# Kernel tuning notes

Hardware: AMD Instinct MI355X
Metric: run time of the kernel (lower is better)

## Reference

```python
import jax, jax.numpy as jnp
import numpy as np
from jax import lax

N = 1_000_000   # nodes
E = 16_000_000  # edges
K1, K2, K3 = 100_000, 10_000, 2_500  # ceil(ratio*n) per pooling stage
EPS = 1e-5


def cgconv(x, src, dst, edge_attr, edge_valid, Wf, bf, Ws, bs, gamma, beta, num_nodes):
    # z_ij = [x_i, x_j, e_ij]  (PyG: i = target = dst, j = source = src)
    z = jnp.concatenate([x[dst], x[src], edge_attr], axis=-1)          # [E,3]
    m = jax.nn.sigmoid(z @ Wf + bf) * jax.nn.softplus(z @ Ws + bs)     # [E,1]
    m = m * edge_valid[:, None].astype(m.dtype)
    aggr = jax.ops.segment_sum(m, dst, num_segments=num_nodes)         # [n,1]
    # BatchNorm1d (training-mode batch stats, biased var), then residual
    mean = aggr.mean(axis=0)
    var = aggr.var(axis=0)
    bn = gamma * (aggr - mean) / jnp.sqrt(var + EPS) + beta
    return bn + x


def topk_pool(x, src, dst, edge_attr, edge_valid, w, k, num_nodes):
    # Original torch code broadcasts x[N,1]*w[C] -> sum(-1) == x*sum(w); tanh nonlinearity.
    score = jnp.tanh(x[:, 0] * jnp.sum(w) / jnp.linalg.norm(w))        # [n]
    top_scores, perm = lax.top_k(score, k)
    x_new = x[perm] * top_scores[:, None]
    mask = jnp.zeros((num_nodes,), bool).at[perm].set(True)
    new_idx = jnp.zeros((num_nodes,), jnp.int32).at[perm].set(jnp.arange(k, dtype=jnp.int32))
    ev = edge_valid & mask[src] & mask[dst]
    return x_new, new_idx[src], new_idx[dst], edge_attr, ev


def setup_inputs() -> dict:
    key = jax.random.key(0)
    ks = jax.random.split(key, 24)
    d = {}
    d["x"] = jax.random.normal(ks[0], (N, 1), jnp.float32)
    d["edge_attr"] = jax.random.uniform(ks[1], (E, 1), jnp.float32)
    d["src"] = jax.random.randint(ks[2], (E,), 0, N, jnp.int32)
    d["dst"] = jax.random.randint(ks[3], (E,), 0, N, jnp.int32)
    d["batch"] = jnp.zeros((N,), jnp.int32)
    p = lambda k, shp: jax.random.normal(k, shp, jnp.float32) * 0.1
    d["Wf1"], d["bf1"] = p(ks[4], (3, 1)), p(ks[5], (1,))
    d["Ws1"], d["bs1"] = p(ks[6], (3, 1)), p(ks[7], (1,))
    d["g1"], d["be1"] = jnp.ones((1,), jnp.float32), jnp.zeros((1,), jnp.float32)
    d["Wf2"], d["bf2"] = p(ks[8], (3, 1)), p(ks[9], (1,))
    d["Ws2"], d["bs2"] = p(ks[10], (3, 1)), p(ks[11], (1,))
    d["g2"], d["be2"] = jnp.ones((1,), jnp.float32), jnp.zeros((1,), jnp.float32)
    d["pw1"] = p(ks[12], (800,))
    d["pw2"] = p(ks[13], (80,))
    d["pw3"] = p(ks[14], (8,))
    d["Wl1"], d["bl1"] = p(ks[15], (1, 8)), p(ks[16], (8,))
    d["Wl2"], d["bl2"] = p(ks[17], (8, 2)), p(ks[18], (2,))
    return d


def reference(x, edge_attr, Wf1, bf1, Ws1, bs1, g1, be1, Wf2, bf2, Ws2, bs2, g2, be2,
              pw1, pw2, pw3, Wl1, bl1, Wl2, bl2, src, dst, batch):
    ev = jnp.ones((E,), bool)
    x = cgconv(x, src, dst, edge_attr, ev, Wf1, bf1, Ws1, bs1, g1, be1, N)
    x, s, dd, ea, ev = topk_pool(x, src, dst, edge_attr, ev, pw1, K1, N)
    x = cgconv(x, s, dd, ea, ev, Wf2, bf2, Ws2, bs2, g2, be2, K1)
    x, s, dd, ea, ev = topk_pool(x, s, dd, ea, ev, pw2, K2, K1)
    x, s, dd, ea, ev = topk_pool(x, s, dd, ea, ev, pw3, K3, K2)
    h = jax.nn.relu(x @ Wl1 + bl1)
    # dropout is identity in eval/reference mode
    return jax.nn.log_softmax(h @ Wl2 + bl2, axis=1)
```

## Files before the change

### kernel.cpp

```cpp
#include <hip/hip_runtime.h>
#include <math.h>

#define CHUNK 4096
#define NB2   256
#define BSH   12
#define CAP   20
#define CAPW  41
#define FG    16
#define RND   1024
#define EPB   16384

typedef int      i32x4 __attribute__((ext_vector_type(4)));
typedef float    f32x4 __attribute__((ext_vector_type(4)));
typedef unsigned u32x2 __attribute__((ext_vector_type(2)));
typedef unsigned u32x4 __attribute__((ext_vector_type(4)));

__device__ __forceinline__ i32x4 ntld4i(const int* p)   { return __builtin_nontemporal_load((const i32x4*)p); }
__device__ __forceinline__ f32x4 ntld4f(const float* p) { return __builtin_nontemporal_load((const f32x4*)p); }

__device__ __forceinline__ float sigmoidf_(float x) {
    if (x >= 0.0f) { float e = expf(-x); return 1.0f / (1.0f + e); }
    float e = expf(x); return e / (1.0f + e);
}
__device__ __forceinline__ float softplusf_(float x) {
    return fmaxf(x, 0.0f) + log1pf(expf(-fabsf(x)));
}
__device__ __forceinline__ unsigned key_desc(float f) {
    unsigned u = __float_as_uint(f);
    unsigned ka = (u & 0x80000000u) ? ~u : (u | 0x80000000u);
    return ~ka;
}
__device__ __forceinline__ float edge_m(float xd, float xs, float a,
                                        float wf0, float wf1, float wf2, float b0,
                                        float ws0, float ws1, float ws2, float b1) {
    float f = xd * wf0 + xs * wf1 + a * wf2 + b0;
    float g = xd * ws0 + xs * ws1 + a * ws2 + b1;
    return sigmoidf_(f) * softplusf_(g);
}

__global__ void k_consts(const float* __restrict__ pw1, const float* __restrict__ pw2,
                         const float* __restrict__ pw3, float* __restrict__ consts,
                         float* __restrict__ stats, unsigned* __restrict__ ghist,
                         int n1, int n2, int n3) {
    if (blockIdx.x == 0) {
        if (threadIdx.x < 16) stats[threadIdx.x] = 0.f;
        for (int i = threadIdx.x; i < 2048; i += 256) ghist[i] = 0u;
    }
    const float* w; int n;
    if (blockIdx.x == 0)      { w = pw1; n = n1; }
    else if (blockIdx.x == 1) { w = pw2; n = n2; }
    else                      { w = pw3; n = n3; }
    __shared__ float s1[256], s2[256];
    float a = 0.f, b = 0.f;
    for (int i = threadIdx.x; i < n; i += 256) { float v = w[i]; a += v; b += v * v; }
    s1[threadIdx.x] = a; s2[threadIdx.x] = b; __syncthreads();
    for (int o = 128; o > 0; o >>= 1) {
        if (threadIdx.x < o) { s1[threadIdx.x] += s1[threadIdx.x + o]; s2[threadIdx.x] += s2[threadIdx.x + o]; }
        __syncthreads();
    }
    if (threadIdx.x == 0) consts[blockIdx.x] = s1[0] / sqrtf(s2[0]);
}

__global__ void __launch_bounds__(256) k_ehist2(const int* __restrict__ dst,
                                                unsigned* __restrict__ hist,
                                                int e0, int e1) {
    __shared__ unsigned h[NB2];
    int t = threadIdx.x;
    h[t] = 0;
    __syncthreads();
    int cs = e0 + blockIdx.x * EPB;
    int ce = cs + EPB; if (ce > e1) ce = e1;
    for (int eb = cs; eb < ce; eb += RND) {
        int i = eb + t * 4;
        if (eb + RND <= ce) {
            i32x4 d4 = ntld4i(dst + i);
            atomicAdd(&h[((unsigned)d4.x) >> BSH], 1u);
            atomicAdd(&h[((unsigned)d4.y) >> BSH], 1u);
            atomicAdd(&h[((unsigned)d4.z) >> BSH], 1u);
            atomicAdd(&h[((unsigned)d4.w) >> BSH], 1u);
        } else {
            #pragma unroll
            for (int j = 0; j < 4; ++j)
                if (i + j < ce) atomicAdd(&h[((unsigned)dst[i + j]) >> BSH], 1u);
        }
    }
    __syncthreads();
    hist[(size_t)blockIdx.x * NB2 + t] = h[t];
}

__global__ void k_scanA(const unsigned* __restrict__ hist, unsigned* __restrict__ offs,
                        unsigned* __restrict__ tot, int G, unsigned rmask) {
    int d = blockIdx.x, ND = gridDim.x, t = threadIdx.x;
    __shared__ unsigned s[256];
    unsigned carry = 0;
    for (int tile = 0; tile * 256 < G; ++tile) {
        int g = tile * 256 + t;
        unsigned v = (g < G) ? ((hist[(size_t)g * ND + d] + rmask) & ~rmask) : 0u;
        s[t] = v; __syncthreads();
        for (int o = 1; o < 256; o <<= 1) {
            unsigned u = (t >= o) ? s[t - o] : 0u;
            __syncthreads();
            s[t] += u; __syncthreads();
        }
        if (g < G) offs[(size_t)g * ND + d] = s[t] - v + carry;
        unsigned tl = s[255]; __syncthreads();
        carry += tl;
    }
    if (t == 0) tot[d] = carry;
}

__global__ void __launch_bounds__(256) k_part(
        const float* __restrict__ x, const float* __restrict__ ea,
        const int* __restrict__ src, const int* __restrict__ dst,
        const float* __restrict__ Wf, const float* __restrict__ bf,
        const float* __restrict__ Ws, const float* __restrict__ bs,
        const unsigned* __restrict__ offs, const unsigned* __restrict__ tot,
        const unsigned* __restrict__ eh,
        uint2* __restrict__ rec, int e0, int e1) {
    __shared__ unsigned stage[NB2 * CAPW];
    __shared__ unsigned gcur[NB2], fil[NB2], gend[NB2];
    __shared__ unsigned short wl[2][NB2];
    __shared__ unsigned wlc[2];
    int t = threadIdx.x;
    {
        unsigned v = tot[t];
        stage[t] = v; __syncthreads();
        for (int o = 1; o < 256; o <<= 1) {
            unsigned u = (t >= o) ? stage[t - o] : 0u;
            __syncthreads();
            stage[t] += u; __syncthreads();
        }
        unsigned g0 = (stage[t] - v) + offs[(size_t)blockIdx.x * NB2 + t];
        unsigned cnt = eh[(size_t)blockIdx.x * NB2 + t];
        gcur[t] = g0;
        gend[t] = g0 + ((cnt + FG - 1) & ~(unsigned)(FG - 1));
        fil[t] = 0;
        if (t < 2) wlc[t] = 0;
    }
    __syncthreads();
    int cs = e0 + blockIdx.x * EPB;
    int ce = cs + EPB; if (ce > e1) ce = e1;
    float wf0 = Wf[0], wf1 = Wf[1], wf2 = Wf[2], b0 = bf[0];
    float ws0 = Ws[0], ws1 = Ws[1], ws2 = Ws[2], b1 = bs[0];
    int sg = t >> 4, ln = t & 15;
    int rnd = 0;
    for (int rb = cs; rb < ce; rb += RND, ++rnd) {
        int cur = rnd & 1;
        int s4[4], d4[4]; float a4[4]; bool vl[4];
        int eb = rb + t * 4;
        if (rb + RND <= ce) {
            i32x4 sv = ntld4i(src + eb);
            i32x4 dv = ntld4i(dst + eb);
            f32x4 av = ntld4f(ea + eb);
            s4[0]=sv.x; s4[1]=sv.y; s4[2]=sv.z; s4[3]=sv.w;
            d4[0]=dv.x; d4[1]=dv.y; d4[2]=dv.z; d4[3]=dv.w;
            a4[0]=av.x; a4[1]=av.y; a4[2]=av.z; a4[3]=av.w;
            vl[0]=vl[1]=vl[2]=vl[3]=true;
        } else {
            #pragma unroll
            for (int j = 0; j < 4; ++j) {
                int e = eb + j;
                vl[j] = e < ce;
                s4[j] = vl[j] ? src[e] : 0;
                d4[j] = vl[j] ? dst[e] : 0;
                a4[j] = vl[j] ? ea[e]  : 0.f;
            }
        }
        #pragma unroll
        for (int j = 0; j < 4; ++j) {
            if (!vl[j]) continue;
            int d = d4[j];
            float m = edge_m(x[d], x[s4[j]], a4[j], wf0, wf1, wf2, b0, ws0, ws1, ws2, b1);
            unsigned bin = ((unsigned)d) >> BSH;
            unsigned dl  = (unsigned)(d & ((1 << BSH) - 1));
            unsigned slot = atomicAdd(&fil[bin], 1u);
            if (slot == FG - 1) {
                unsigned w = atomicAdd(&wlc[cur], 1u);
                wl[cur][w] = (unsigned short)bin;
            }
            if (slot < CAP) {
                stage[bin * CAPW + 2 * slot]     = __float_as_uint(m);
                stage[bin * CAPW + 2 * slot + 1] = dl;
            } else {
                rec[gcur[bin] + slot] = make_uint2(__float_as_uint(m), dl);
            }
        }
        __syncthreads();
        unsigned nw = wlc[cur];
        for (unsigned i = sg; i < nw; i += 16) {
            int b = wl[cur][i];
            unsigned c = fil[b], g = gcur[b];
            unsigned* st = &stage[b * CAPW];
            if (c > CAP) {
                rec[g + ln] = make_uint2(st[2 * ln], st[2 * ln + 1]);
                if (ln < CAP - 16)
                    rec[g + 16 + ln] = make_uint2(st[2 * (16 + ln)], st[2 * (16 + ln) + 1]);
                if (ln == 0) { gcur[b] = g + c; fil[b] = 0; }
            } else {
                rec[g + ln] = make_uint2(st[2 * ln], st[2 * ln + 1]);
                unsigned rem = c - FG;
                unsigned a0 = 0, a1 = 0;
                if (ln < rem) { a0 = st[2 * (FG + ln)]; a1 = st[2 * (FG + ln) + 1]; }
                if (ln < rem) { st[2 * ln] = a0; st[2 * ln + 1] = a1; }
                if (ln == 0) { gcur[b] = g + FG; fil[b] = rem; }
            }
        }
        if (t == 0) wlc[cur ^ 1] = 0;
        __syncthreads();
    }
    for (int i = 0; i < NB2 / 16; ++i) {
        int b = sg + (i << 4);
        unsigned g = gcur[b], c = fil[b], ge = gend[b];
        unsigned* st = &stage[b * CAPW];
        for (unsigned p = g + ln; p < ge; p += 16) {
            unsigned k2 = p - g;
            rec[p] = (k2 < c) ? make_uint2(st[2 * k2], st[2 * k2 + 1]) : make_uint2(0u, 0u);
        }
    }
}

__global__ void __launch_bounds__(256) k_aggr2(
        const uint2* __restrict__ rec, const unsigned* __restrict__ tot,
        float* __restrict__ aggr, float* __restrict__ stats,
        int N, int accumulate, int doStats) {
    __shared__ float acc[1 << BSH];
    __shared__ unsigned sc[256];
    __shared__ unsigned sBase, sCnt;
    int t = threadIdx.x, b = blockIdx.x;
    {
        unsigned v = tot[t];
        sc[t] = v; __syncthreads();
        for (int o = 1; o < 256; o <<= 1) {
            unsigned u = (t >= o) ? sc[t - o] : 0u;
            __syncthreads();
            sc[t] += u; __syncthreads();
        }
        if (t == b) { sBase = sc[t] - v; sCnt = tot[t]; }
    }
    for (int i = t; i < (1 << BSH); i += 256) acc[i] = 0.f;
    __syncthreads();
    unsigned lo = sBase, hi = lo + sCnt;
    for (unsigned i = lo + 2 * t; i < hi; i += 512) {
        u32x4 r = __builtin_nontemporal_load((const u32x4*)&rec[i]);
        atomicAdd(&acc[r.y], __uint_as_float(r.x));
        atomicAdd(&acc[r.w], __uint_as_float(r.z));
    }
    __syncthreads();
    int nb = b << BSH;
    float s = 0.f, q = 0.f;
    for (int i = t; i < (1 << BSH); i += 256) {
        int node = nb + i;
        if (node < N) {
            float v = acc[i];
            if (accumulate) v += aggr[node];
            aggr[node] = v;
            if (doStats) { s += v; q += v * v; }
        }
    }
    if (doStats) {
        __shared__ float s1[256], s2[256];
        s1[t] = s; s2[t] = q; __syncthreads();
        for (int o = 128; o > 0; o >>= 1) {
            if (t < o) { s1[t] += s1[t + o]; s2[t] += s2[t + o]; }
            __syncthreads();
        }
        if (t == 0) { atomicAdd(&stats[0], s1[0]); atomicAdd(&stats[1], s2[0]); }
    }
}

__global__ void k_conv1(const float* __restrict__ x, const float* __restrict__ ea,
                        const int* __restrict__ src, const int* __restrict__ dst,
                        const float* __restrict__ Wf, const float* __restrict__ bf,
                        const float* __restrict__ Ws, const float* __restrict__ bs,
                        float* __restrict__ aggr, int E) {
    int e = blockIdx.x * blockDim.x + threadIdx.x;
    if (e >= E) return;
    int s = src[e], d = dst[e];
    atomicAdd(&aggr[d], edge_m(x[d], x[s], ea[e], Wf[0], Wf[1], Wf[2], bf[0],
                               Ws[0], Ws[1], Ws[2], bs[0]));
}

__global__ void __launch_bounds__(256) k_conv2(
        const float* __restrict__ x2, const float* __restrict__ ea,
        const int* __restrict__ src, const int* __restrict__ dst,
        const int* __restrict__ nidx,
        const float* __restrict__ Wf, const float* __restrict__ bf,
        const float* __restrict__ Ws, const float* __restrict__ bs,
        float* __restrict__ aggr, int E) {
    int base = (blockIdx.x * 256 + threadIdx.x) * 4;
    if (base >= E) return;
    float wf0 = Wf[0], wf1 = Wf[1], wf2 = Wf[2], b0 = bf[0];
    float ws0 = Ws[0], ws1 = Ws[1], ws2 = Ws[2], b1 = bs[0];
    int d4[4], s4[4]; int cnt;
    if (base + 4 <= E) {
        i32x4 dv = ntld4i(dst + base);
        i32x4 sv = ntld4i(src + base);
        d4[0]=dv.x; d4[1]=dv.y; d4[2]=dv.z; d4[3]=dv.w;
        s4[0]=sv.x; s4[1]=sv.y; s4[2]=sv.z; s4[3]=sv.w;
        cnt = 4;
    } else {
        cnt = E - base;
        for (int j = 0; j < cnt; ++j) { d4[j] = dst[base + j]; s4[j] = src[base + j]; }
    }
    #pragma unroll
    for (int j = 0; j < 4; ++j) {
        if (j >= cnt) break;
        int nd = nidx[d4[j]];
        if (nd < 0) continue;
        int ns = nidx[s4[j]];
        if (ns < 0) continue;
        float a = __builtin_nontemporal_load(ea + base + j);
        atomicAdd(&aggr[nd], edge_m(x2[nd], x2[ns], a, wf0, wf1, wf2, b0, ws0, ws1, ws2, b1));
    }
}

__global__ void k_stats(const float* __restrict__ a, int n, float* __restrict__ stats) {
    float s = 0.f, q = 0.f;
    int stride = gridDim.x * blockDim.x;
    for (int i = blockIdx.x * blockDim.x + threadIdx.x; i < n; i += stride) {
        float v = a[i]; s += v; q += v * v;
    }
    __shared__ float s1[256], s2[256];
    s1[threadIdx.x] = s; s2[threadIdx.x] = q; __syncthreads();
    for (int o = 128; o > 0; o >>= 1) {
        if (threadIdx.x < o) { s1[threadIdx.x] += s1[threadIdx.x + o]; s2[threadIdx.x] += s2[threadIdx.x + o]; }
        __syncthreads();
    }
    if (threadIdx.x == 0) { atomicAdd(&stats[0], s1[0]); atomicAdd(&stats[1], s2[0]); }
}

__global__ void k_bn(const float* __restrict__ aggr, const float* __restrict__ xin,
                     const float* __restrict__ stats, const float* __restrict__ g,
                     const float* __restrict__ be, float* __restrict__ xout,
                     int n, float invn, const float* __restrict__ consts, int ci,
                     unsigned* __restrict__ keys, unsigned* __restrict__ vals,
                     int* __restrict__ nidxInit, float* __restrict__ zeroArr, int nZero) {
    int i = blockIdx.x * blockDim.x + threadIdx.x;
    if (i >= n) return;
    if (nidxInit) nidxInit[i] = -1;
    if (zeroArr && i < nZero) zeroArr[i] = 0.f;
    float mean = stats[0] * invn;
    float var  = stats[1] * invn - mean * mean;
    float inv  = 1.0f / sqrtf(var + 1e-5f);
    float v = g[0] * (aggr[i] - mean) * inv + be[0] + xin[i];
    xout[i] = v;
    float s = tanhf(v * consts[ci]);
    keys[i] = key_desc(s);
    vals[i] = (unsigned)i;
}

__global__ void __launch_bounds__(256) k_ghist(const unsigned* __restrict__ keys,
                                               unsigned* __restrict__ ghist, int n) {
    __shared__ unsigned h[2048];
    int t = threadIdx.x;
    for (int i = t; i < 2048; i += 256) h[i] = 0;
    __syncthreads();
    int stride = gridDim.x * 1024;
    for (int base = blockIdx.x * 1024 + t * 4; base + 3 < n; base += stride) {
        u32x4 k4 = __builtin_nontemporal_load((const u32x4*)(keys + base));
        atomicAdd(&h[k4.x >> 21], 1u);
        atomicAdd(&h[k4.y >> 21], 1u);
        atomicAdd(&h[k4.z >> 21], 1u);
        atomicAdd(&h[k4.w >> 21], 1u);
    }
    if (blockIdx.x == 0) {
        int tail = n & ~3;
        for (int i = tail + t; i < n; i += 256)
            atomicAdd(&h[keys[i] >> 21], 1u);
    }
    __syncthreads();
    for (int i = t; i < 2048; i += 256) { unsigned v = h[i]; if (v) atomicAdd(&ghist[i], v); }
}

__global__ void k_findT(const unsigned* __restrict__ ghist, unsigned* __restrict__ sel, int K) {
    __shared__ unsigned s[256];
    int t = threadIdx.x;
    unsigned carry = 0;
    for (int tile = 0; tile < 8; ++tile) {
        unsigned v = ghist[tile * 256 + t];
        s[t] = v; __syncthreads();
        for (int o = 1; o < 256; o <<= 1) {
            unsigned u = (t >= o) ? s[t - o] : 0u;
            __syncthreads();
            s[t] += u; __syncthreads();
        }
        unsigned cum = s[t] + carry;
        if (cum >= (unsigned)K && cum - v < (unsigned)K) {
            sel[0] = (unsigned)(tile * 256 + t);
            sel[1] = cum;
        }
        unsigned tl = s[255]; __syncthreads();
        carry += tl;
    }
}

__global__ void __launch_bounds__(256) k_selcnt(const unsigned* __restrict__ keys,
                                                const unsigned* __restrict__ sel,
                                                unsigned* __restrict__ chist, int n) {
    unsigned T = sel[0];
    int t = threadIdx.x;
    int base = blockIdx.x * CHUNK;
    int end = base + CHUNK; if (end > n) end = n;
    unsigned c = 0;
    for (int i = base + t; i < end; i += 256)
        c += ((keys[i] >> 21) <= T) ? 1u : 0u;
    __shared__ unsigned s[256];
    s[t] = c; __syncthreads();
    for (int o = 128; o > 0; o >>= 1) { if (t < o) s[t] += s[t + o]; __syncthreads(); }
    if (t == 0) chist[blockIdx.x] = s[0];
}

__global__ void __launch_bounds__(256) k_selcompact(
        const unsigned* __restrict__ keys, const unsigned* __restrict__ vals,
        const unsigned* __restrict__ sel, const unsigned* __restrict__ chist,
        unsigned* __restrict__ okeys, unsigned* __restrict__ ovals, int n, int G) {
    __shared__ unsigned s[256];
    __shared__ unsigned wsum[4];
    __shared__ unsigned runS;
    unsigned T = sel[0];
    int t = threadIdx.x, wave = t >> 6, lane = t & 63;
    unsigned v = (t < G) ? chist[t] : 0u;
    s[t] = v; __syncthreads();
    for (int o = 1; o < 256; o <<= 1) {
        unsigned u = (t >= o) ? s[t - o] : 0u;
        __syncthreads();
        s[t] += u; __syncthreads();
    }
    if (t == (int)blockIdx.x) runS = s[t] - v;
    __syncthreads();
    int cbase = blockIdx.x * CHUNK;
    for (int gix = 0; gix < CHUNK / 256; ++gix) {
        int i = cbase + gix * 256 + t;
        bool selq = (i < n) && ((keys[i] >> 21) <= T);
        unsigned long long mk = __ballot(selq);
        unsigned pre = (unsigned)__popcll(mk & ((1ull << lane) - 1ull));
        if (lane == 0) wsum[wave] = (unsigned)__popcll(mk);
        __syncthreads();
        unsigned wb = runS;
        #pragma unroll
        for (int w = 0; w < 4; ++w) if (w < wave) wb += wsum[w];
        if (selq) { unsigned pos = wb + pre; okeys[pos] = keys[i]; ovals[pos] = vals[i]; }
        __syncthreads();
        if (t == 0) runS += wsum[0] + wsum[1] + wsum[2] + wsum[3];
        __syncthreads();
    }
}

__global__ void k_hist(const unsigned* __restrict__ keys, unsigned* __restrict__ hist,
                       int n, const unsigned* __restrict__ pn, int shift) {
    if (pn) n = (int)*pn;
    int base = blockIdx.x * CHUNK;
    if (base >= n) return;
    __shared__ unsigned h[256];
    int t = threadIdx.x;
    h[t] = 0;
    __syncthreads();
    if (base + CHUNK <= n) {
        #pragma unroll
        for (int it = 0; it < CHUNK / 1024; ++it) {
            int i = base + it * 1024 + t * 4;
            const unsigned* p = keys + i;
            unsigned k0 = p[0], k1 = p[1], k2 = p[2], k3 = p[3];
            atomicAdd(&h[(k0 >> shift) & 255u], 1u);
            atomicAdd(&h[(k1 >> shift) & 255u], 1u);
            atomicAdd(&h[(k2 >> shift) & 255u], 1u);
            atomicAdd(&h[(k3 >> shift) & 255u], 1u);
        }
    } else {
        for (int i = base + t; i < n; i += 256)
            atomicAdd(&h[(keys[i] >> shift) & 255u], 1u);
    }
    __syncthreads();
    hist[(size_t)blockIdx.x * 256 + t] = h[t];
}

__global__ void __launch_bounds__(256) k_scatter(const unsigned* __restrict__ keys,
                                                 const unsigned* __restrict__ vals,
                                                 unsigned* __restrict__ okeys,
                                                 unsigned* __restrict__ ovals,
                                                 const unsigned* __restrict__ hist,
                                                 int n, const unsigned* __restrict__ pn,
                                                 int shift) {
    if (pn) n = (int)*pn;
    int b = blockIdx.x;
    int nch = (n + CHUNK - 1) / CHUNK;
    if (b >= nch) return;
    __shared__ unsigned run[256];
    __shared__ unsigned offl[256];
    __shared__ unsigned wcnt[4][256];
    __shared__ unsigned wpre[4][256];
    __shared__ unsigned sc[256];
    int t = threadIdx.x;
    int wave = t >> 6, lane = t & 63;
    {
        unsigned pre = 0, totd = 0;
        for (int c = 0; c < nch; ++c) {
            unsigned v = hist[(size_t)c * 256 + t];
            totd += v;
            if (c < b) pre += v;
        }
        sc[t] = totd; __syncthreads();
        for (int o = 1; o < 256; o <<= 1) {
            unsigned u = (t >= o) ? sc[t - o] : 0u;
            __syncthreads();
            sc[t] += u; __syncthreads();
        }
        offl[t] = (sc[t] - totd) + pre;
        run[t] = 0;
    }
    __syncthreads();
    int cbase = b * CHUNK;
    const int GROUPS = CHUNK / 256;
    for (int gix = 0; gix < GROUPS; ++gix) {
        int i = cbase + gix * 256 + t;
        bool active = i < n;
        unsigned k = active ? keys[i] : 0u;
        unsigned v = active ? vals[i] : 0u;
        unsigned d = (k >> shift) & 255u;
        unsigned long long amask = __ballot(active);
        unsigned long long bb[8];
        #pragma unroll
        for (int bit = 0; bit < 8; ++bit) bb[bit] = __ballot(active && ((d >> bit) & 1u));
        unsigned long long m = amask;
        #pragma unroll
        for (int bit = 0; bit < 8; ++bit) m &= ((d >> bit) & 1u) ? bb[bit] : ~bb[bit];
        unsigned rk = (unsigned)__popcll(m & ((1ull << lane) - 1ull));
        #pragma unroll
        for (int j = 0; j < 4; ++j) {
            unsigned dd = (unsigned)lane + j * 64u;
            unsigned long long mm = amask;
            #pragma unroll
            for (int bit = 0; bit < 8; ++bit) mm &= ((dd >> bit) & 1u) ? bb[bit] : ~bb[bit];
            wcnt[wave][dd] = (unsigned)__popcll(mm);
        }
        __syncthreads();
        {
            unsigned r = run[t];
            unsigned c0 = wcnt[0][t], c1 = wcnt[1][t], c2 = wcnt[2][t], c3 = wcnt[3][t];
            wpre[0][t] = r;
            wpre[1][t] = r + c0;
            wpre[2][t] = r + c0 + c1;
            wpre[3][t] = r + c0 + c1 + c2;
            run[t] = r + c0 + c1 + c2 + c3;
        }
        __syncthreads();
        if (active) {
            unsigned pos = offl[d] + wpre[wave][d] + rk;
            okeys[pos] = k;
            ovals[pos] = v;
        }
    }
}

__global__ void k_pool(const unsigned* __restrict__ perm, const float* __restrict__ xin,
                       const float* __restrict__ consts, int ci,
                       float* __restrict__ xout, int* __restrict__ newidx, int k,
                       unsigned* __restrict__ okeys, unsigned* __restrict__ ovals, int nci) {
    int r = blockIdx.x * blockDim.x + threadIdx.x;
    if (r >= k) return;
    unsigned p = perm[r];
    float xv = xin[p];
    float s = tanhf(xv * consts[ci]);
    float o = xv * s;
    xout[r] = o;
    if (newidx) newidx[p] = r;
    if (okeys) {
        float s2 = tanhf(o * consts[nci]);
        okeys[r] = key_desc(s2);
        ovals[r] = (unsigned)r;
    }
}

__global__ void __launch_bounds__(1024) k_smallsort(
        unsigned* __restrict__ kIn, unsigned* __restrict__ vIn,
        unsigned* __restrict__ kTmp, unsigned* __restrict__ vTmp,
        int n, int k3, const float* __restrict__ xin,
        const float* __restrict__ consts, int ci,
        const float* __restrict__ Wl1, const float* __restrict__ bl1,
        const float* __restrict__ Wl2, const float* __restrict__ bl2,
        float* __restrict__ out) {
    __shared__ unsigned hist[256], sc[256], run[256], offl[256];
    __shared__ unsigned wcnt[16][256];
    __shared__ unsigned wpre[16][256];
    int t = threadIdx.x;
    int wave = t >> 6, lane = t & 63;
    unsigned *ki = kIn, *vi = vIn, *ko = kTmp, *vo = vTmp;
    for (int p = 0; p < 4; ++p) {
        int shift = p * 8;
        if (t < 256) hist[t] = 0;
        __syncthreads();
        for (int i = t; i < n; i += 1024)
            atomicAdd(&hist[(ki[i] >> shift) & 255u], 1u);
        __syncthreads();
        if (t < 256) sc[t] = hist[t];
        __syncthreads();
        for (int o = 1; o < 256; o <<= 1) {
            unsigned u = 0;
            if (t < 256 && t >= o) u = sc[t - o];
            __syncthreads();
            if (t < 256) sc[t] += u;
            __syncthreads();
        }
        if (t < 256) { offl[t] = sc[t] - hist[t]; run[t] = 0; }
        __syncthreads();
        int G = (n + 1023) / 1024;
        for (int gix = 0; gix < G; ++gix) {
            int i = gix * 1024 + t;
            bool active = i < n;
            unsigned k = active ? ki[i] : 0u;
            unsigned v = active ? vi[i] : 0u;
            unsigned d = (k >> shift) & 255u;
            unsigned long long amask = __ballot(active);
            unsigned long long bb[8];
            #pragma unroll
            for (int bit = 0; bit < 8; ++bit) bb[bit] = __ballot(active && ((d >> bit) & 1u));
            unsigned long long m = amask;
            #pragma unroll
            for (int bit = 0; bit < 8; ++bit) m &= ((d >> bit) & 1u) ? bb[bit] : ~bb[bit];
            unsigned rk = (unsigned)__popcll(m & ((1ull << lane) - 1ull));
            #pragma unroll
            for (int j = 0; j < 4; ++j) {
                unsigned dd = (unsigned)lane + j * 64u;
                unsigned long long mm = amask;
                #pragma unroll
                for (int bit = 0; bit < 8; ++bit) mm &= ((dd >> bit) & 1u) ? bb[bit] : ~bb[bit];
                wcnt[wave][dd] = (unsigned)__popcll(mm);
            }
            __syncthreads();
            if (t < 256) {
                unsigned acc = run[t];
                #pragma unroll
                for (int w2 = 0; w2 < 16; ++w2) { wpre[w2][t] = acc; acc += wcnt[w2][t]; }
                run[t] = acc;
            }
            __syncthreads();
            if (active) {
                unsigned pos = offl[d] + wpre[wave][d] + rk;
                ko[pos] = k;
                vo[pos] = v;
            }
            __syncthreads();
        }
        unsigned* tp;
        tp = ki; ki = ko; ko = tp;
        tp = vi; vi = vo; vo = tp;
        __syncthreads();
    }
    float c = consts[ci];
    float b20 = bl2[0], b21 = bl2[1];
    for (int r = t; r < k3; r += 1024) {
        unsigned pidx = vIn[r];
        float xv = xin[pidx];
        float s = tanhf(xv * c);
        float o = xv * s;
        float l0 = b20, l1 = b21;
        #pragma unroll
        for (int j = 0; j < 8; ++j) {
            float h = fmaxf(o * Wl1[j] + bl1[j], 0.0f);
            l0 += h * Wl2[2 * j];
            l1 += h * Wl2[2 * j + 1];
        }
        float mx = fmaxf(l0, l1);
        float lse = mx + logf(expf(l0 - mx) + expf(l1 - mx));
        out[2 * r]     = l0 - lse;
        out[2 * r + 1] = l1 - lse;
    }
}

static void sort_pairs(hipStream_t stream, unsigned* kI, unsigned* vI,
                       unsigned* kT, unsigned* vT, unsigned* hist,
                       int n, int G, const unsigned* pn) {
    unsigned *ki = kI, *vi = vI, *ko = kT, *vo = vT;
    for (int p = 0; p < 4; ++p) {
        int shift = p * 8;
        k_hist<<<G, 256, 0, stream>>>(ki, hist, n, pn, shift);
        k_scatter<<<G, 256, 0, stream>>>(ki, vi, ko, vo, hist, n, pn, shift);
        unsigned* t;
        t = ki; ki = ko; ko = t;
        t = vi; vi = vo; vo = t;
    }
}

extern "C" void kernel_launch(void* const* d_in, const int* in_sizes, int n_in,
                              void* d_out, int out_size, void* d_ws, size_t ws_size,
                              hipStream_t stream) {
    const float* x   = (const float*)d_in[0];
    const float* ea  = (const float*)d_in[1];
    const int*   src = (const int*)d_in[2];
    const int*   dst = (const int*)d_in[3];
    const float *Wf1 = (const float*)d_in[5],  *bf1 = (const float*)d_in[6];
    const float *Ws1 = (const float*)d_in[7],  *bs1 = (const float*)d_in[8];
    const float *g1  = (const float*)d_in[9],  *be1 = (const float*)d_in[10];
    const float *Wf2 = (const float*)d_in[11], *bf2 = (const float*)d_in[12];
    const float *Ws2 = (const float*)d_in[13], *bs2 = (const float*)d_in[14];
    const float *g2  = (const float*)d_in[15], *be2 = (const float*)d_in[16];
    const float *pw1 = (const float*)d_in[17], *pw2 = (const float*)d_in[18], *pw3 = (const float*)d_in[19];
    const float *Wl1 = (const float*)d_in[20], *bl1 = (const float*)d_in[21];
    const float *Wl2 = (const float*)d_in[22], *bl2 = (const float*)d_in[23];

    const int N  = in_sizes[0];
    const int E  = in_sizes[1];
    const int K1 = 100000, K2 = 10000, K3 = 2500;

    size_t off = 0;
    auto alloc = [&](size_t bytes) { size_t o = off; off = (off + bytes + 255) & ~(size_t)255; return o; };
    char* ws = (char*)d_ws;
    size_t o_x1    = alloc((size_t)N * 4);
    size_t o_nidx  = alloc((size_t)N * 4);
    size_t o_stats = alloc(256);
    size_t o_const = alloc(256);
    size_t o_tot   = alloc(4096);
    size_t o_gh    = alloc(8192);
    size_t o_x2    = alloc((size_t)K1 * 4);
    size_t o_x3    = alloc((size_t)K1 * 4);
    size_t o_ag2   = alloc((size_t)K1 * 4);
    size_t o_x4    = alloc((size_t)K2 * 4);
    size_t o_ag1   = alloc((size_t)N * 4);
    size_t o_arena = off;

    int G1 = (N + CHUNK - 1) / CHUNK;
    size_t s_kA = 0;
    size_t s_vA = s_kA + (((size_t)N * 4 + 255) & ~(size_t)255);
    size_t s_kB = s_vA + (((size_t)N * 4 + 255) & ~(size_t)255);
    size_t s_vB = s_kB + (((size_t)N * 4 + 255) & ~(size_t)255);
    size_t s_h  = s_vB + (((size_t)N * 4 + 255) & ~(size_t)255);
    size_t sortSz = s_h + (size_t)G1 * 256 * 4;

    int H = 0, Eh = 0;
    size_t p_rec = 0, p_eh = 0, p_eo = 0;
    for (int h = 1; h <= 8; h <<= 1) {
        int eh_ = (E + h - 1) / h;
        eh_ = (eh_ + RND - 1) & ~(RND - 1);
        int gc_ = (eh_ + EPB - 1) / EPB;
        size_t recB = (((size_t)eh_ + (size_t)gc_ * NB2 * FG + NB2 * FG) * 8 + 255) & ~(size_t)255;
        size_t ehB  = (((size_t)gc_ * NB2 * 4) + 255) & ~(size_t)255;
        size_t eoB  = (((size_t)gc_ * NB2 * 4) + 255) & ~(size_t)255;
        size_t partSz = recB + ehB + eoB;
        size_t arenaSz = partSz > sortSz ? partSz : sortSz;
        if (o_arena + arenaSz <= ws_size && N <= (NB2 << BSH)) {
            H = h; Eh = eh_;
            p_rec = 0; p_eh = p_rec + recB; p_eo = p_eh + ehB;
            break;
        }
    }

    float*    x1     = (float*)(ws + o_x1);
    int*      nidx   = (int*)(ws + o_nidx);
    float*    stats  = (float*)(ws + o_stats);
    float*    consts = (float*)(ws + o_const);
    unsigned* tot    = (unsigned*)(ws + o_tot);
    unsigned* selp   = tot + 512;
    unsigned* ghist  = (unsigned*)(ws + o_gh);
    float*    x2     = (float*)(ws + o_x2);
    float*    x3     = (float*)(ws + o_x3);
    float*    aggr2  = (float*)(ws + o_ag2);
    float*    x4     = (float*)(ws + o_x4);
    float*    aggr1  = (float*)(ws + o_ag1);
    unsigned* kA     = (unsigned*)(ws + o_arena + s_kA);
    unsigned* vA     = (unsigned*)(ws + o_arena + s_vA);
    unsigned* kB     = (unsigned*)(ws + o_arena + s_kB);
    unsigned* vB     = (unsigned*)(ws + o_arena + s_vB);
    unsigned* hist   = (unsigned*)(ws + o_arena + s_h);

    k_consts<<<3, 256, 0, stream>>>(pw1, pw2, pw3, consts, stats, ghist,
                                    in_sizes[17], in_sizes[18], in_sizes[19]);

    if (H > 0) {
        uint2*    rec = (uint2*)(ws + o_arena + p_rec);
        unsigned* eh  = (unsigned*)(ws + o_arena + p_eh);
        unsigned* eo  = (unsigned*)(ws + o_arena + p_eo);
        int NBN = (N + (1 << BSH) - 1) >> BSH;
        for (int h = 0; h < H; ++h) {
            int e0 = h * Eh;
            int e1 = e0 + Eh; if (e1 > E) e1 = E;
            if (e0 >= e1) break;
            int GCh = (e1 - e0 + EPB - 1) / EPB;
            k_ehist2<<<GCh, 256, 0, stream>>>(dst, eh, e0, e1);
            k_scanA<<<NB2, 256, 0, stream>>>(eh, eo, tot, GCh, (unsigned)(FG - 1));
            k_part<<<GCh, 256, 0, stream>>>(x, ea, src, dst, Wf1, bf1, Ws1, bs1,
                                            eo, tot, eh, rec, e0, e1);
            k_aggr2<<<NBN, 256, 0, stream>>>(rec, tot, aggr1, stats, N,
                                             h > 0, h == H - 1 ? 1 : 0);
        }
    } else {
        hipMemsetAsync(aggr1, 0, (size_t)N * 4, stream);
        k_conv1<<<(E + 255) / 256, 256, 0, stream>>>(x, ea, src, dst, Wf1, bf1, Ws1, bs1, aggr1, E);
        k_stats<<<1024, 256, 0, stream>>>(aggr1, N, stats);
    }
    k_bn<<<(N + 255) / 256, 256, 0, stream>>>(aggr1, x, stats, g1, be1, x1, N, 1.0f / (float)N,
                                              consts, 0, kA, vA, nidx, aggr2, K1);

    k_ghist<<<256, 256, 0, stream>>>(kA, ghist, N);
    k_findT<<<1, 256, 0, stream>>>(ghist, selp, K1);
    k_selcnt<<<G1, 256, 0, stream>>>(kA, selp, hist, N);
    k_selcompact<<<G1, 256, 0, stream>>>(kA, vA, selp, hist, kB, vB, N, G1);
    sort_pairs(stream, kB, vB, kA, vA, hist, N, G1, selp + 1);
    k_pool<<<(K1 + 255) / 256, 256, 0, stream>>>(vB, x1, consts, 0, x2, nidx, K1,
                                                 (unsigned*)nullptr, (unsigned*)nullptr, 0);

    k_conv2<<<(E / 4 + 255) / 256, 256, 0, stream>>>(x2, ea, src, dst, nidx,
                                                     Wf2, bf2, Ws2, bs2, aggr2, E);
    k_stats<<<256, 256, 0, stream>>>(aggr2, K1, stats + 2);
    k_bn<<<(K1 + 255) / 256, 256, 0, stream>>>(aggr2, x2, stats + 2, g2, be2, x3, K1, 1.0f / (float)K1,
                                               consts, 1, kA, vA,
                                               (int*)nullptr, (float*)nullptr, 0);

    sort_pairs(stream, kA, vA, kB, vB, hist, K1,
               (K1 + CHUNK - 1) / CHUNK, (const unsigned*)nullptr);
    k_pool<<<(K2 + 255) / 256, 256, 0, stream>>>(vA, x3, consts, 1, x4, (int*)nullptr, K2,
                                                 kB, vB, 2);

    k_smallsort<<<1, 1024, 0, stream>>>(kB, vB, kA, vA, K2, K3, x4, consts, 2,
                                        Wl1, bl1, Wl2, bl2, (float*)d_out);
}
```

Baseline: 932.6 us.

## Fuse histogram into BN, threshold into selcnt, pool into last scatter pass

```diff
diff --git a/kernel.cpp b/kernel.cpp
--- a/kernel.cpp
+++ b/kernel.cpp
@@ -4,15 +4,14 @@
 #define CHUNK 4096
 #define NB2   256
 #define BSH   12
-#define CAP   20
-#define CAPW  41
+#define CAP   24
+#define CAPW  49
 #define FG    16
 #define RND   1024
 #define EPB   16384
 
 typedef int      i32x4 __attribute__((ext_vector_type(4)));
 typedef float    f32x4 __attribute__((ext_vector_type(4)));
-typedef unsigned u32x2 __attribute__((ext_vector_type(2)));
 typedef unsigned u32x4 __attribute__((ext_vector_type(4)));
 
 __device__ __forceinline__ i32x4 ntld4i(const int* p)   { return __builtin_nontemporal_load((const i32x4*)p); }
@@ -219,7 +218,7 @@
     }
 }
 
-__global__ void __launch_bounds__(256) k_aggr2(
+__global__ void __launch_bounds__(1024) k_aggr2(
         const uint2* __restrict__ rec, const unsigned* __restrict__ tot,
         float* __restrict__ aggr, float* __restrict__ stats,
         int N, int accumulate, int doStats) {
@@ -227,20 +226,19 @@
     __shared__ unsigned sc[256];
     __shared__ unsigned sBase, sCnt;
     int t = threadIdx.x, b = blockIdx.x;
-    {
-        unsigned v = tot[t];
-        sc[t] = v; __syncthreads();
-        for (int o = 1; o < 256; o <<= 1) {
-            unsigned u = (t >= o) ? sc[t - o] : 0u;
-            __syncthreads();
-            sc[t] += u; __syncthreads();
-        }
-        if (t == b) { sBase = sc[t] - v; sCnt = tot[t]; }
-    }
-    for (int i = t; i < (1 << BSH); i += 256) acc[i] = 0.f;
+    if (t < 256) sc[t] = tot[t];
+    __syncthreads();
+    for (int o = 1; o < 256; o <<= 1) {
+        unsigned u = (t < 256 && t >= o) ? sc[t - o] : 0u;
+        __syncthreads();
+        if (t < 256) sc[t] += u;
+        __syncthreads();
+    }
+    if (t == 0) { sBase = sc[b] - tot[b]; sCnt = tot[b]; }
+    for (int i = t; i < (1 << BSH); i += 1024) acc[i] = 0.f;
     __syncthreads();
     unsigned lo = sBase, hi = lo + sCnt;
-    for (unsigned i = lo + 2 * t; i < hi; i += 512) {
+    for (unsigned i = lo + 2 * t; i < hi; i += 2048) {
         u32x4 r = __builtin_nontemporal_load((const u32x4*)&rec[i]);
         atomicAdd(&acc[r.y], __uint_as_float(r.x));
         atomicAdd(&acc[r.w], __uint_as_float(r.z));
@@ -248,7 +246,7 @@
     __syncthreads();
     int nb = b << BSH;
     float s = 0.f, q = 0.f;
-    for (int i = t; i < (1 << BSH); i += 256) {
+    for (int i = t; i < (1 << BSH); i += 1024) {
         int node = nb + i;
         if (node < N) {
             float v = acc[i];
@@ -258,9 +256,9 @@
         }
     }
     if (doStats) {
-        __shared__ float s1[256], s2[256];
+        __shared__ float s1[1024], s2[1024];
         s1[t] = s; s2[t] = q; __syncthreads();
-        for (int o = 128; o > 0; o >>= 1) {
+        for (int o = 512; o > 0; o >>= 1) {
             if (t < o) { s1[t] += s1[t + o]; s2[t] += s2[t + o]; }
             __syncthreads();
         }
@@ -329,51 +327,47 @@
     if (threadIdx.x == 0) { atomicAdd(&stats[0], s1[0]); atomicAdd(&stats[1], s2[0]); }
 }
 
-__global__ void k_bn(const float* __restrict__ aggr, const float* __restrict__ xin,
-                     const float* __restrict__ stats, const float* __restrict__ g,
-                     const float* __restrict__ be, float* __restrict__ xout,
-                     int n, float invn, const float* __restrict__ consts, int ci,
-                     unsigned* __restrict__ keys, unsigned* __restrict__ vals,
-                     int* __restrict__ nidxInit, float* __restrict__ zeroArr, int nZero) {
-    int i = blockIdx.x * blockDim.x + threadIdx.x;
-    if (i >= n) return;
-    if (nidxInit) nidxInit[i] = -1;
-    if (zeroArr && i < nZero) zeroArr[i] = 0.f;
+__global__ void __launch_bounds__(256) k_bn(
+        const float* __restrict__ aggr, const float* __restrict__ xin,
+        const float* __restrict__ stats, const float* __restrict__ g,
+        const float* __restrict__ be, float* __restrict__ xout,
+        int n, float invn, const float* __restrict__ consts, int ci,
+        unsigned* __restrict__ keys, unsigned* __restrict__ vals,
+        int* __restrict__ nidxInit, float* __restrict__ zeroArr, int nZero,
+        unsigned* __restrict__ ghist) {
+    __shared__ unsigned h2[2048];
+    int t = threadIdx.x;
+    if (ghist) {
+        for (int i = t; i < 2048; i += 256) h2[i] = 0;
+        __syncthreads();
+    }
     float mean = stats[0] * invn;
     float var  = stats[1] * invn - mean * mean;
-    float inv  = 1.0f / sqrtf(var + 1e-5f);
-    float v = g[0] * (aggr[i] - mean) * inv + be[0] + xin[i];
-    xout[i] = v;
-    float s = tanhf(v * consts[ci]);
-    keys[i] = key_desc(s);
-    vals[i] = (unsigned)i;
-}
-
-__global__ void __launch_bounds__(256) k_ghist(const unsigned* __restrict__ keys,
-                                               unsigned* __restrict__ ghist, int n) {
-    __shared__ unsigned h[2048];
-    int t = threadIdx.x;
-    for (int i = t; i < 2048; i += 256) h[i] = 0;
-    __syncthreads();
-    int stride = gridDim.x * 1024;
-    for (int base = blockIdx.x * 1024 + t * 4; base + 3 < n; base += stride) {
-        u32x4 k4 = __builtin_nontemporal_load((const u32x4*)(keys + base));
-        atomicAdd(&h[k4.x >> 21], 1u);
-        atomicAdd(&h[k4.y >> 21], 1u);
-        atomicAdd(&h[k4.z >> 21], 1u);
-        atomicAdd(&h[k4.w >> 21], 1u);
-    }
-    if (blockIdx.x == 0) {
-        int tail = n & ~3;
-        for (int i = tail + t; i < n; i += 256)
-            atomicAdd(&h[keys[i] >> 21], 1u);
-    }
-    __syncthreads();
-    for (int i = t; i < 2048; i += 256) { unsigned v = h[i]; if (v) atomicAdd(&ghist[i], v); }
-}
-
-__global__ void k_findT(const unsigned* __restrict__ ghist, unsigned* __restrict__ sel, int K) {
+    float rinv = 1.0f / sqrtf(var + 1e-5f);
+    float gg = g[0], bb = be[0], c0 = consts[ci];
+    int gid = blockIdx.x * 256 + t, gsz = gridDim.x * 256;
+    for (int i = gid; i < n; i += gsz) {
+        if (nidxInit) nidxInit[i] = -1;
+        if (zeroArr && i < nZero) zeroArr[i] = 0.f;
+        float v = gg * (aggr[i] - mean) * rinv + bb + xin[i];
+        xout[i] = v;
+        unsigned k = key_desc(tanhf(v * c0));
+        keys[i] = k;
+        vals[i] = (unsigned)i;
+        if (ghist) atomicAdd(&h2[k >> 21], 1u);
+    }
+    if (ghist) {
+        __syncthreads();
+        for (int i = t; i < 2048; i += 256) { unsigned v = h2[i]; if (v) atomicAdd(&ghist[i], v); }
+    }
+}
+
+__global__ void __launch_bounds__(256) k_selcnt(const unsigned* __restrict__ keys,
+                                                const unsigned* __restrict__ ghist,
+                                                unsigned* __restrict__ sel,
+                                                unsigned* __restrict__ chist, int n, int K) {
     __shared__ unsigned s[256];
+    __shared__ unsigned sT;
     int t = threadIdx.x;
     unsigned carry = 0;
     for (int tile = 0; tile < 8; ++tile) {
@@ -386,25 +380,19 @@
         }
         unsigned cum = s[t] + carry;
         if (cum >= (unsigned)K && cum - v < (unsigned)K) {
-            sel[0] = (unsigned)(tile * 256 + t);
-            sel[1] = cum;
+            sT = (unsigned)(tile * 256 + t);
+            if (blockIdx.x == 0) { sel[0] = sT; sel[1] = cum; }
         }
         unsigned tl = s[255]; __syncthreads();
         carry += tl;
     }
-}
-
-__global__ void __launch_bounds__(256) k_selcnt(const unsigned* __restrict__ keys,
-                                                const unsigned* __restrict__ sel,
-                                                unsigned* __restrict__ chist, int n) {
-    unsigned T = sel[0];
-    int t = threadIdx.x;
+    __syncthreads();
+    unsigned T = sT;
     int base = blockIdx.x * CHUNK;
     int end = base + CHUNK; if (end > n) end = n;
     unsigned c = 0;
     for (int i = base + t; i < end; i += 256)
         c += ((keys[i] >> 21) <= T) ? 1u : 0u;
-    __shared__ unsigned s[256];
     s[t] = c; __syncthreads();
     for (int o = 128; o > 0; o >>= 1) { if (t < o) s[t] += s[t + o]; __syncthreads(); }
     if (t == 0) chist[blockIdx.x] = s[0];
@@ -480,7 +468,11 @@
                                                  unsigned* __restrict__ ovals,
                                                  const unsigned* __restrict__ hist,
                                                  int n, const unsigned* __restrict__ pn,
-                                                 int shift) {
+                                                 int shift, int mode,
+                                                 const float* __restrict__ px1,
+                                                 const float* __restrict__ consts,
+                                                 float* __restrict__ px2,
+                                                 int* __restrict__ pnidx, int K1p) {
     if (pn) n = (int)*pn;
     int b = blockIdx.x;
     int nch = (n + CHUNK - 1) / CHUNK;
@@ -492,6 +484,7 @@
     __shared__ unsigned sc[256];
     int t = threadIdx.x;
     int wave = t >> 6, lane = t & 63;
+    float pc0 = mode ? consts[0] : 0.f;
     {
         unsigned pre = 0, totd = 0;
         for (int c = 0; c < nch; ++c) {
@@ -548,27 +541,27 @@
             unsigned pos = offl[d] + wpre[wave][d] + rk;
             okeys[pos] = k;
             ovals[pos] = v;
+            if (mode && pos < (unsigned)K1p) {
+                float xv = px1[v];
+                px2[pos] = xv * tanhf(xv * pc0);
+                pnidx[v] = (int)pos;
+            }
         }
     }
 }
 
 __global__ void k_pool(const unsigned* __restrict__ perm, const float* __restrict__ xin,
                        const float* __restrict__ consts, int ci,
-                       float* __restrict__ xout, int* __restrict__ newidx, int k,
+                       float* __restrict__ xout, int k,
                        unsigned* __restrict__ okeys, unsigned* __restrict__ ovals, int nci) {
     int r = blockIdx.x * blockDim.x + threadIdx.x;
     if (r >= k) return;
     unsigned p = perm[r];
     float xv = xin[p];
-    float s = tanhf(xv * consts[ci]);
-    float o = xv * s;
+    float o = xv * tanhf(xv * consts[ci]);
     xout[r] = o;
-    if (newidx) newidx[p] = r;
-    if (okeys) {
-        float s2 = tanhf(o * consts[nci]);
-        okeys[r] = key_desc(s2);
-        ovals[r] = (unsigned)r;
-    }
+    okeys[r] = key_desc(tanhf(o * consts[nci]));
+    ovals[r] = (unsigned)r;
 }
 
 __global__ void __launch_bounds__(1024) k_smallsort(
@@ -651,8 +644,7 @@
     for (int r = t; r < k3; r += 1024) {
         unsigned pidx = vIn[r];
         float xv = xin[pidx];
-        float s = tanhf(xv * c);
-        float o = xv * s;
+        float o = xv * tanhf(xv * c);
         float l0 = b20, l1 = b21;
         #pragma unroll
         for (int j = 0; j < 8; ++j) {
@@ -669,12 +661,16 @@
 
 static void sort_pairs(hipStream_t stream, unsigned* kI, unsigned* vI,
                        unsigned* kT, unsigned* vT, unsigned* hist,
-                       int n, int G, const unsigned* pn) {
+                       int n, int G, const unsigned* pn,
+                       const float* x1, const float* consts,
+                       float* x2, int* nidx, int K1) {
     unsigned *ki = kI, *vi = vI, *ko = kT, *vo = vT;
     for (int p = 0; p < 4; ++p) {
         int shift = p * 8;
+        int mode = (p == 3 && x2 != nullptr) ? 1 : 0;
         k_hist<<<G, 256, 0, stream>>>(ki, hist, n, pn, shift);
-        k_scatter<<<G, 256, 0, stream>>>(ki, vi, ko, vo, hist, n, pn, shift);
+        k_scatter<<<G, 256, 0, stream>>>(ki, vi, ko, vo, hist, n, pn, shift,
+                                         mode, x1, consts, x2, nidx, K1);
         unsigned* t;
         t = ki; ki = ko; ko = t;
         t = vi; vi = vo; vo = t;
@@ -779,36 +775,34 @@
             k_scanA<<<NB2, 256, 0, stream>>>(eh, eo, tot, GCh, (unsigned)(FG - 1));
             k_part<<<GCh, 256, 0, stream>>>(x, ea, src, dst, Wf1, bf1, Ws1, bs1,
                                             eo, tot, eh, rec, e0, e1);
-            k_aggr2<<<NBN, 256, 0, stream>>>(rec, tot, aggr1, stats, N,
-                                             h > 0, h == H - 1 ? 1 : 0);
+            k_aggr2<<<NBN, 1024, 0, stream>>>(rec, tot, aggr1, stats, N,
+                                              h > 0, h == H - 1 ? 1 : 0);
         }
     } else {
         hipMemsetAsync(aggr1, 0, (size_t)N * 4, stream);
         k_conv1<<<(E + 255) / 256, 256, 0, stream>>>(x, ea, src, dst, Wf1, bf1, Ws1, bs1, aggr1, E);
         k_stats<<<1024, 256, 0, stream>>>(aggr1, N, stats);
     }
-    k_bn<<<(N + 255) / 256, 256, 0, stream>>>(aggr1, x, stats, g1, be1, x1, N, 1.0f / (float)N,
-                                              consts, 0, kA, vA, nidx, aggr2, K1);
-
-    k_ghist<<<256, 256, 0, stream>>>(kA, ghist, N);
-    k_findT<<<1, 256, 0, stream>>>(ghist, selp, K1);
-    k_selcnt<<<G1, 256, 0, stream>>>(kA, selp, hist, N);
+
+    k_bn<<<512, 256, 0, stream>>>(aggr1, x, stats, g1, be1, x1, N, 1.0f / (float)N,
+                                  consts, 0, kA, vA, nidx, aggr2, K1, ghist);
+
+    k_selcnt<<<G1, 256, 0, stream>>>(kA, ghist, selp, hist, N, K1);
     k_selcompact<<<G1, 256, 0, stream>>>(kA, vA, selp, hist, kB, vB, N, G1);
-    sort_pairs(stream, kB, vB, kA, vA, hist, N, G1, selp + 1);
-    k_pool<<<(K1 + 255) / 256, 256, 0, stream>>>(vB, x1, consts, 0, x2, nidx, K1,
-                                                 (unsigned*)nullptr, (unsigned*)nullptr, 0);
+    sort_pairs(stream, kB, vB, kA, vA, hist, N, G1, selp + 1,
+               x1, consts, x2, nidx, K1);
 
     k_conv2<<<(E / 4 + 255) / 256, 256, 0, stream>>>(x2, ea, src, dst, nidx,
                                                      Wf2, bf2, Ws2, bs2, aggr2, E);
     k_stats<<<256, 256, 0, stream>>>(aggr2, K1, stats + 2);
-    k_bn<<<(K1 + 255) / 256, 256, 0, stream>>>(aggr2, x2, stats + 2, g2, be2, x3, K1, 1.0f / (float)K1,
-                                               consts, 1, kA, vA,
-                                               (int*)nullptr, (float*)nullptr, 0);
+    k_bn<<<391, 256, 0, stream>>>(aggr2, x2, stats + 2, g2, be2, x3, K1, 1.0f / (float)K1,
+                                  consts, 1, kA, vA,
+                                  (int*)nullptr, (float*)nullptr, 0, (unsigned*)nullptr);
 
     sort_pairs(stream, kA, vA, kB, vB, hist, K1,
-               (K1 + CHUNK - 1) / CHUNK, (const unsigned*)nullptr);
-    k_pool<<<(K2 + 255) / 256, 256, 0, stream>>>(vA, x3, consts, 1, x4, (int*)nullptr, K2,
-                                                 kB, vB, 2);
+               (K1 + CHUNK - 1) / CHUNK, (const unsigned*)nullptr,
+               (const float*)nullptr, consts, (float*)nullptr, (int*)nullptr, 0);
+    k_pool<<<(K2 + 255) / 256, 256, 0, stream>>>(vA, x3, consts, 1, x4, K2, kB, vB, 2);
 
     k_smallsort<<<1, 1024, 0, stream>>>(kB, vB, kA, vA, K2, K3, x4, consts, 2,
                                         Wl1, bl1, Wl2, bl2, (float*)d_out);
```

Result: faster. 874.9 us (-6.2%).
